# Optimization experiments

Measured on AMD Instinct MI355X. Metric: run time of the kernel, lower is better.

## Reference

```python
import jax, jax.numpy as jnp
import numpy as np

B, S, D, H, E, K = 1, 2048, 1024, 16, 8, 2
DK = D // H          # 64 per-head key dim
FF = 4 * D           # 4096 expert hidden
EPS = 1e-5


def rmsnorm(x, scale):
    rms = jnp.sqrt(jnp.mean(x * x, axis=-1, keepdims=True) + EPS)
    return scale * (x / rms)


def setup_inputs() -> dict:
    key = jax.random.key(0)
    ks = jax.random.split(key, 12)
    std = 0.02
    x = jax.random.normal(ks[0], (B, S, D), dtype=jnp.float32)
    # causal mask: masked_fill where mask == 0
    self_attn_mask = jnp.tril(jnp.ones((S, S), dtype=jnp.int32))
    scale_attn = jnp.ones((D,), dtype=jnp.float32)
    scale_ffn = jnp.ones((D,), dtype=jnp.float32)
    # per-head projections, stacked: [H, DK, D] (torch Linear weight layout [out,in])
    Wq = jax.random.normal(ks[1], (H, DK, D), dtype=jnp.float32) * std
    Wk = jax.random.normal(ks[2], (H, DK, D), dtype=jnp.float32) * std
    Wv = jax.random.normal(ks[3], (H, DK, D), dtype=jnp.float32) * std
    Wo = jax.random.normal(ks[4], (D, D), dtype=jnp.float32) * std
    Wg = jax.random.normal(ks[5], (E, D), dtype=jnp.float32) * std   # router gate
    W_in = jax.random.normal(ks[6], (E, FF, D), dtype=jnp.float32) * std   # expert linear
    W_v = jax.random.normal(ks[7], (E, FF, D), dtype=jnp.float32) * std    # expert linear_v
    W_out = jax.random.normal(ks[8], (E, D, FF), dtype=jnp.float32) * std  # expert linear_out
    return {
        'x': x, 'self_attn_mask': self_attn_mask,
        'scale_attn': scale_attn, 'Wq': Wq, 'Wk': Wk, 'Wv': Wv, 'Wo': Wo,
        'scale_ffn': scale_ffn, 'Wg': Wg, 'W_in': W_in, 'W_v': W_v, 'W_out': W_out,
    }


def reference(x, self_attn_mask, scale_attn, Wq, Wk, Wv, Wo, scale_ffn, Wg, W_in, W_v, W_out):
    # --- self attention (pre-RMSNorm) ---
    normed = rmsnorm(x, scale_attn)
    q = jnp.einsum('bsd,hkd->bhsk', normed, Wq)
    k = jnp.einsum('bsd,hkd->bhsk', normed, Wk)
    v = jnp.einsum('bsd,hkd->bhsk', normed, Wv)
    attn = jnp.einsum('bhsk,bhtk->bhst', q, k) / np.sqrt(DK).astype(np.float32)
    attn = jnp.where(self_attn_mask[None, None] == 0, -jnp.inf, attn)
    attn = jax.nn.softmax(attn, axis=-1)
    ctx = jnp.einsum('bhst,bhtk->bhsk', attn, v)
    ctx = ctx.transpose(0, 2, 1, 3).reshape(x.shape[0], x.shape[1], D)  # concat heads
    a1 = ctx @ Wo.T
    x = x + a1
    # --- MoE (pre-RMSNorm) ---
    normed = rmsnorm(x, scale_ffn)
    router_logits = normed @ Wg.T                       # [B,S,E]
    router_probs = jax.nn.softmax(router_logits, axis=-1)
    gate, idx = jax.lax.top_k(router_probs, K)          # [B,S,K]
    gate = gate / jnp.sum(gate, axis=-1, keepdims=True)
    # combine weights per expert: sum of renormalized gates over selected slots
    onehot = (idx[..., None] == jnp.arange(E)).astype(x.dtype)  # [B,S,K,E]
    combine = jnp.sum(gate[..., None] * onehot, axis=2)         # [B,S,E]
    # all-expert dense FFN (faithful to the masked dense loop in torch)
    g = jax.nn.gelu(jnp.einsum('bsd,efd->bsef', normed, W_in), approximate=False)
    val = jnp.einsum('bsd,efd->bsef', normed, W_v)
    eo = jnp.einsum('bsef,edf->bsed', g * val, W_out)           # [B,S,E,D]
    moe_out = jnp.einsum('bse,bsed->bsd', combine, eo)
    out = x + moe_out
    return (out, router_probs)
```

## Files before the change

### kernel.cpp

```cpp
#include <hip/hip_runtime.h>
#include <hip/hip_bf16.h>
#include <math.h>

typedef unsigned int u32;
typedef unsigned short u16;
using bf16x8 = __attribute__((ext_vector_type(8))) short;
using f32x4 = __attribute__((ext_vector_type(4))) float;

#define MFMA_BF16(a, b, c) __builtin_amdgcn_mfma_f32_16x16x32_bf16((a), (b), (c), 0, 0, 0)
#define VMCNT8() asm volatile("s_waitcnt vmcnt(8)" ::: "memory")
#define VMCNT6() asm volatile("s_waitcnt vmcnt(6)" ::: "memory")
#define VMCNT4() asm volatile("s_waitcnt vmcnt(4)" ::: "memory")
#define VMCNT0() asm volatile("s_waitcnt vmcnt(0)" ::: "memory")
#define SBAR() __builtin_amdgcn_s_barrier()
#define SCHED0() __builtin_amdgcn_sched_barrier(0)

constexpr int kS = 2048, kD = 1024, kH = 16, kE = 8, kFF = 4096;
constexpr int kSlotCap = 5120;
constexpr int kMaxTiles = 40;
constexpr int kChunk = 8;

__device__ __forceinline__ u16 bf16_rne(float f) {
  u32 u = __float_as_uint(f);
  u32 r = (u + 0x7fffu + ((u >> 16) & 1u)) >> 16;
  return (u16)r;
}
__device__ __forceinline__ float bf16_f32(u16 h) { return __uint_as_float(((u32)h) << 16); }
__device__ __forceinline__ u32 pack_hl(float x) {
  u16 hi = bf16_rne(x);
  u16 lo = bf16_rne(x - bf16_f32(hi));
  return ((u32)lo << 16) | (u32)hi;
}
__device__ __forceinline__ void unpack8(const u32* t, bf16x8& h, bf16x8& l) {
#pragma unroll
  for (int j = 0; j < 8; j++) {
    h[j] = (short)(t[j] & 0xffffu);
    l[j] = (short)(t[j] >> 16);
  }
}
__device__ __forceinline__ void gload_lds16(const void* g, void* l) {
  __builtin_amdgcn_global_load_lds((const __attribute__((address_space(1))) u32*)g,
                                   (__attribute__((address_space(3))) u32*)l, 16, 0, 0);
}
__device__ __forceinline__ u32 cvtpk(float a, float b) {
  u32 r;
  asm("v_cvt_pk_bf16_f32 %0, %1, %2" : "=v"(r) : "v"(a), "v"(b));
  return r;
}

__global__ __launch_bounds__(256) void pack_dp3(const float* __restrict__ Wq,
                                                const float* __restrict__ Wk,
                                                const float* __restrict__ Wv,
                                                u16* __restrict__ o) {
  int i = blockIdx.x * 256 + threadIdx.x;
  if (i >= 3072 * 1024) return;
  int n = i >> 10, k = i & 1023;
  float v = (n < 1024) ? Wq[i] : (n < 2048) ? Wk[i - 1024 * 1024] : Wv[i - 2048 * 1024];
  u16 hi = bf16_rne(v);
  u16 lo = bf16_rne(v - bf16_f32(hi));
  size_t b = (size_t)n * 2048 + (size_t)(k >> 5) * 64 + (k & 31);
  o[b] = hi;
  o[b + 32] = lo;
}
__global__ __launch_bounds__(256) void pack_dp1(const float* __restrict__ W,
                                                u16* __restrict__ o, int n_elem) {
  int i = blockIdx.x * 256 + threadIdx.x;
  if (i >= n_elem) return;
  int k = i & 1023, n = i >> 10;
  float v = W[i];
  u16 hi = bf16_rne(v);
  u16 lo = bf16_rne(v - bf16_f32(hi));
  size_t b = (size_t)n * 2048 + (size_t)(k >> 5) * 64 + (k & 31);
  o[b] = hi;
  o[b + 32] = lo;
}

template <int MODE>
__global__ __launch_bounds__(256) void rmsnorm_kernel(
    const float* __restrict__ x, const float* __restrict__ scale,
    u16* __restrict__ odp, float* __restrict__ of32, u16* __restrict__ ob16) {
  const int s = blockIdx.x;
  const float* row = x + (size_t)s * kD;
  const int c = threadIdx.x * 4;
  float4 v = *(const float4*)(row + c);
  float ss = v.x * v.x + v.y * v.y + v.z * v.z + v.w * v.w;
#pragma unroll
  for (int m = 32; m; m >>= 1) ss += __shfl_xor(ss, m);
  __shared__ float wsum[4];
  if ((threadIdx.x & 63) == 0) wsum[threadIdx.x >> 6] = ss;
  __syncthreads();
  float tot = wsum[0] + wsum[1] + wsum[2] + wsum[3];
  float rinv = 1.0f / sqrtf(tot * (1.0f / kD) + 1e-5f);
  float4 sc = *(const float4*)(scale + c);
  float n[4] = {v.x * rinv * sc.x, v.y * rinv * sc.y, v.z * rinv * sc.z, v.w * rinv * sc.w};
  if (MODE == 0) {
    u16 hv[4], lv[4];
#pragma unroll
    for (int j = 0; j < 4; j++) {
      hv[j] = bf16_rne(n[j]);
      lv[j] = bf16_rne(n[j] - bf16_f32(hv[j]));
    }
    u16* o = odp + (size_t)s * 2048 + (size_t)(c >> 5) * 64 + (c & 31);
    *(uint2*)o = *(uint2*)hv;
    *(uint2*)(o + 32) = *(uint2*)lv;
  } else {
    *(float4*)(of32 + (size_t)s * kD + c) = make_float4(n[0], n[1], n[2], n[3]);
    u16* o = ob16 + (size_t)s * kD + c;
    o[0] = bf16_rne(n[0]); o[1] = bf16_rne(n[1]); o[2] = bf16_rne(n[2]); o[3] = bf16_rne(n[3]);
  }
}

template <int APK, int OUT>
__global__ __launch_bounds__(256) void gemm_dp(
    const void* __restrict__ Av, const u16* __restrict__ Bdp,
    const float* __restrict__ resid, int K,
    u32* __restrict__ oq, u32* __restrict__ ok, u32* __restrict__ ov,
    float* __restrict__ of) {
  __shared__ u16 As[2][128 * 64];
  __shared__ u16 Bs[2][128 * 64];
  const int tid = threadIdx.x, w = tid >> 6, l = tid & 63;
  const int m0 = blockIdx.y * 128, n0 = blockIdx.x * 128;
  const int wr = (w >> 1) * 64, wc = (w & 1) * 64;
  const char* Ab = (const char*)Av;
  const char* Bb = (const char*)Bdp;
  const size_t rowb = (size_t)K * 4;

  size_t asrc[4], bsrc[4];
  int dst[4];
#pragma unroll
  for (int i = 0; i < 4; i++) {
    int fl = i * 256 + tid;
    int row = fl >> 3, cb = fl & 7;
    size_t coff = (size_t)((cb ^ (row & 7)) * 16);
    asrc[i] = (size_t)(m0 + row) * rowb + coff;
    bsrc[i] = (size_t)(n0 + row) * rowb + coff;
    dst[i] = fl * 16;
  }

  f32x4 zero = {0.f, 0.f, 0.f, 0.f};
  f32x4 acc[4][4];
#pragma unroll
  for (int i = 0; i < 4; i++)
#pragma unroll
    for (int j = 0; j < 4; j++) acc[i][j] = zero;

  auto stage = [&](int buf, int s) {
    const char* ap = Ab + (size_t)s * 128;
    const char* bp = Bb + (size_t)s * 128;
#pragma unroll
    for (int i = 0; i < 4; i++) {
      gload_lds16(ap + asrc[i], (char*)&As[buf][0] + dst[i]);
      gload_lds16(bp + bsrc[i], (char*)&Bs[buf][0] + dst[i]);
    }
  };

  const int NS = K / 32;
  stage(0, 0);
  for (int s = 0; s < NS; s++) {
    const int cur = s & 1;
    const bool lastit = (s == NS - 1);
    if (!lastit) stage(cur ^ 1, s + 1);
    if (!lastit) VMCNT8(); else VMCNT0();
    SBAR();
    SCHED0();
    bf16x8 ah[4], al[4], bh[4], bl[4];
    const int g = l >> 4;
    if (APK) {
      const u32* At = (const u32*)&As[cur][0];
#pragma unroll
      for (int mi = 0; mi < 4; mi++) {
        int row = wr + mi * 16 + (l & 15);
        u32 t[8];
        *(uint4*)t = *(const uint4*)&At[row * 32 + (((2 * g) ^ (row & 7)) * 4)];
        *(uint4*)(t + 4) = *(const uint4*)&At[row * 32 + (((2 * g + 1) ^ (row & 7)) * 4)];
        unpack8(t, ah[mi], al[mi]);
      }
    } else {
#pragma unroll
      for (int mi = 0; mi < 4; mi++) {
        int row = wr + mi * 16 + (l & 15);
        ah[mi] = *(const bf16x8*)&As[cur][row * 64 + ((g ^ (row & 7)) * 8)];
        al[mi] = *(const bf16x8*)&As[cur][row * 64 + (((4 + g) ^ (row & 7)) * 8)];
      }
    }
#pragma unroll
    for (int ni = 0; ni < 4; ni++) {
      int row = wc + ni * 16 + (l & 15);
      bh[ni] = *(const bf16x8*)&Bs[cur][row * 64 + ((g ^ (row & 7)) * 8)];
      bl[ni] = *(const bf16x8*)&Bs[cur][row * 64 + (((4 + g) ^ (row & 7)) * 8)];
    }
#pragma unroll
    for (int mi = 0; mi < 4; mi++)
#pragma unroll
      for (int ni = 0; ni < 4; ni++) {
        f32x4 c = acc[mi][ni];
        c = MFMA_BF16(al[mi], bh[ni], c);
        c = MFMA_BF16(ah[mi], bl[ni], c);
        c = MFMA_BF16(ah[mi], bh[ni], c);
        acc[mi][ni] = c;
      }
    SCHED0();
    if (!lastit) SBAR();
  }

  if (OUT == 0) {
    u32* dstp;
    int nb;
    if (n0 < 1024) { dstp = oq; nb = n0; }
    else if (n0 < 2048) { dstp = ok; nb = n0 - 1024; }
    else { dstp = ov; nb = n0 - 2048; }
#pragma unroll
    for (int mi = 0; mi < 4; mi++)
#pragma unroll
      for (int ni = 0; ni < 4; ni++)
#pragma unroll
        for (int r = 0; r < 4; r++) {
          int row = m0 + wr + mi * 16 + ((l >> 4) << 2) + r;
          int col = nb + wc + ni * 16 + (l & 15);
          dstp[(size_t)row * 1024 + col] = pack_hl(acc[mi][ni][r]);
        }
  } else {
#pragma unroll
    for (int mi = 0; mi < 4; mi++)
#pragma unroll
      for (int ni = 0; ni < 4; ni++)
#pragma unroll
        for (int r = 0; r < 4; r++) {
          int row = m0 + wr + mi * 16 + ((l >> 4) << 2) + r;
          int col = n0 + wc + ni * 16 + (l & 15);
          of[(size_t)row * 1024 + col] = resid[(size_t)row * 1024 + col] + acc[mi][ni][r];
        }
  }
}

__global__ __launch_bounds__(256) void attn_kernel(
    const u32* __restrict__ Qp, const u32* __restrict__ Kp, const u32* __restrict__ Vp,
    float* __restrict__ Opart, float* __restrict__ mpart, float* __restrict__ lpart) {
  constexpr int LDK = 68;
  __shared__ u32 Ks[64 * LDK];
  __shared__ u32 Vs[64 * LDK];
  __shared__ u32 Ps[64 * LDK];
  const int tid = threadIdx.x, w = tid >> 6, l = tid & 63;
  int b = blockIdx.x, qt, c;
  if (b < 8) { qt = b; c = 0; }
  else if (b < 24) { qt = 8 + ((b - 8) >> 1); c = (b - 8) & 1; }
  else if (b < 48) { qt = 16 + (b - 24) / 3; c = (b - 24) % 3; }
  else { qt = 24 + ((b - 48) >> 2); c = (b - 48) & 3; }
  const int hh = blockIdx.y;
  const int q0 = qt * 64, hc = hh * 64;
  const int kt0 = c * kChunk;
  const int kt1 = min(kt0 + kChunk, qt + 1);

  bf16x8 qh[2], ql[2];
  {
    const int qrow = q0 + w * 16 + (l & 15);
#pragma unroll
    for (int kk = 0; kk < 2; kk++) {
      u32 t[8];
      const u32* p = Qp + (size_t)qrow * kD + hc + kk * 32 + ((l >> 4) << 3);
      *(uint4*)t = *(const uint4*)p;
      *(uint4*)(t + 4) = *(const uint4*)(p + 4);
      unpack8(t, qh[kk], ql[kk]);
    }
  }
  float mrun[4], lrun[4];
  f32x4 zero = {0.f, 0.f, 0.f, 0.f};
  f32x4 oacc[4];
#pragma unroll
  for (int r = 0; r < 4; r++) { mrun[r] = -3.0e38f; lrun[r] = 0.f; }
#pragma unroll
  for (int vb = 0; vb < 4; vb++) oacc[vb] = zero;

  const int trow = tid >> 2, c0v = (tid & 3) * 16;
  const u32* gKb = Kp + hc + c0v;
  const u32* gVb = Vp + hc + c0v;
  uint4 kr[4], vr[4];
  {
    const u32* gK = gKb + (size_t)(kt0 * 64 + trow) * kD;
    kr[0] = *(const uint4*)gK; kr[1] = *(const uint4*)(gK + 4);
    kr[2] = *(const uint4*)(gK + 8); kr[3] = *(const uint4*)(gK + 12);
    const u32* gV = gVb + (size_t)(kt0 * 64 + trow) * kD;
    vr[0] = *(const uint4*)gV; vr[1] = *(const uint4*)(gV + 4);
    vr[2] = *(const uint4*)(gV + 8); vr[3] = *(const uint4*)(gV + 12);
  }

  for (int kt = kt0; kt < kt1; kt++) {
    {
      u32* sK = Ks + trow * LDK + c0v;
      *(uint4*)sK = kr[0]; *(uint4*)(sK + 4) = kr[1];
      *(uint4*)(sK + 8) = kr[2]; *(uint4*)(sK + 12) = kr[3];
#pragma unroll
      for (int j = 0; j < 4; j++) {
        Vs[(c0v + j * 4 + 0) * LDK + trow] = vr[j].x;
        Vs[(c0v + j * 4 + 1) * LDK + trow] = vr[j].y;
        Vs[(c0v + j * 4 + 2) * LDK + trow] = vr[j].z;
        Vs[(c0v + j * 4 + 3) * LDK + trow] = vr[j].w;
      }
    }
    __syncthreads();
    if (kt + 1 < kt1) {
      const u32* gK = gKb + (size_t)((kt + 1) * 64 + trow) * kD;
      kr[0] = *(const uint4*)gK; kr[1] = *(const uint4*)(gK + 4);
      kr[2] = *(const uint4*)(gK + 8); kr[3] = *(const uint4*)(gK + 12);
      const u32* gV = gVb + (size_t)((kt + 1) * 64 + trow) * kD;
      vr[0] = *(const uint4*)gV; vr[1] = *(const uint4*)(gV + 4);
      vr[2] = *(const uint4*)(gV + 8); vr[3] = *(const uint4*)(gV + 12);
    }

    f32x4 sfr[4];
#pragma unroll
    for (int kb = 0; kb < 4; kb++) {
      f32x4 sa = zero;
#pragma unroll
      for (int kk = 0; kk < 2; kk++) {
        u32 t[8];
        bf16x8 kh, kl;
        const u32* p = Ks + (kb * 16 + (l & 15)) * LDK + kk * 32 + ((l >> 4) << 3);
        *(uint4*)t = *(const uint4*)p;
        *(uint4*)(t + 4) = *(const uint4*)(p + 4);
        unpack8(t, kh, kl);
        sa = MFMA_BF16(ql[kk], kl, sa);
        sa = MFMA_BF16(ql[kk], kh, sa);
        sa = MFMA_BF16(qh[kk], kl, sa);
        sa = MFMA_BF16(qh[kk], kh, sa);
      }
      sfr[kb] = sa * 0.125f;
    }
    if (kt == qt) {
#pragma unroll
      for (int kb = 0; kb < 4; kb++) {
        int t = kt * 64 + kb * 16 + (l & 15);
#pragma unroll
        for (int r = 0; r < 4; r++) {
          int qq = q0 + w * 16 + ((l >> 4) << 2) + r;
          if (t > qq) sfr[kb][r] = -3.0e38f;
        }
      }
    }
#pragma unroll
    for (int r = 0; r < 4; r++) {
      float mx = fmaxf(fmaxf(sfr[0][r], sfr[1][r]), fmaxf(sfr[2][r], sfr[3][r]));
#pragma unroll
      for (int mm = 1; mm < 16; mm <<= 1) mx = fmaxf(mx, __shfl_xor(mx, mm));
      float mnew = fmaxf(mrun[r], mx);
      float sf = __expf(mrun[r] - mnew);
      mrun[r] = mnew;
      float rs = 0.f;
#pragma unroll
      for (int kb = 0; kb < 4; kb++) {
        float p = __expf(sfr[kb][r] - mnew);
        sfr[kb][r] = p;
        rs += p;
      }
#pragma unroll
      for (int mm = 1; mm < 16; mm <<= 1) rs += __shfl_xor(rs, mm);
      lrun[r] = lrun[r] * sf + rs;
#pragma unroll
      for (int vb = 0; vb < 4; vb++) oacc[vb][r] *= sf;
    }
#pragma unroll
    for (int kb = 0; kb < 4; kb++)
#pragma unroll
      for (int r = 0; r < 4; r++)
        Ps[(w * 16 + ((l >> 4) << 2) + r) * LDK + kb * 16 + (l & 15)] = pack_hl(sfr[kb][r]);
#pragma unroll
    for (int ks = 0; ks < 2; ks++) {
      bf16x8 ph, pl;
      {
        u32 t[8];
        const u32* pp = Ps + (w * 16 + (l & 15)) * LDK + ks * 32 + ((l >> 4) << 3);
        *(uint4*)t = *(const uint4*)pp;
        *(uint4*)(t + 4) = *(const uint4*)(pp + 4);
        unpack8(t, ph, pl);
      }
#pragma unroll
      for (int vb = 0; vb < 4; vb++) {
        u32 t2[8];
        bf16x8 vh, vl;
        const u32* pv = Vs + (vb * 16 + (l & 15)) * LDK + ks * 32 + ((l >> 4) << 3);
        *(uint4*)t2 = *(const uint4*)pv;
        *(uint4*)(t2 + 4) = *(const uint4*)(pv + 4);
        unpack8(t2, vh, vl);
        f32x4 cc = oacc[vb];
        cc = MFMA_BF16(pl, vl, cc);
        cc = MFMA_BF16(pl, vh, cc);
        cc = MFMA_BF16(ph, vl, cc);
        cc = MFMA_BF16(ph, vh, cc);
        oacc[vb] = cc;
      }
    }
    __syncthreads();
  }

  const int p = (qt * 16 + hh) * 4 + c;
  float* Po = Opart + (size_t)p * 4096;
#pragma unroll
  for (int vb = 0; vb < 4; vb++)
#pragma unroll
    for (int r = 0; r < 4; r++) {
      int rl = w * 16 + ((l >> 4) << 2) + r;
      int cl = vb * 16 + (l & 15);
      Po[rl * 64 + cl] = oacc[vb][r];
    }
  if ((l & 15) == 0) {
#pragma unroll
    for (int r = 0; r < 4; r++) {
      int rl = w * 16 + ((l >> 4) << 2) + r;
      mpart[p * 64 + rl] = mrun[r];
      lpart[p * 64 + rl] = lrun[r];
    }
  }
}

__global__ __launch_bounds__(256) void attn_merge(
    const float* __restrict__ Opart, const float* __restrict__ mpart,
    const float* __restrict__ lpart, u32* __restrict__ Op) {
  const int qt = blockIdx.x, hh = blockIdx.y;
  const int nch = (qt + kChunk) >> 3;
  const int t = threadIdx.x;
  const int row = t >> 2;
  const int c0 = (t & 3) * 16;
  const int pbase = (qt * 16 + hh) * 4;
  float M = -3.0e38f;
  for (int c = 0; c < nch; c++) M = fmaxf(M, mpart[(pbase + c) * 64 + row]);
  float den = 0.f;
  float acc[16];
#pragma unroll
  for (int j = 0; j < 16; j++) acc[j] = 0.f;
  for (int c = 0; c < nch; c++) {
    float wgt = __expf(mpart[(pbase + c) * 64 + row] - M);
    den += wgt * lpart[(pbase + c) * 64 + row];
    const float* po = Opart + (size_t)(pbase + c) * 4096 + row * 64 + c0;
#pragma unroll
    for (int j = 0; j < 16; j += 4) {
      float4 v = *(const float4*)(po + j);
      acc[j] += wgt * v.x; acc[j + 1] += wgt * v.y;
      acc[j + 2] += wgt * v.z; acc[j + 3] += wgt * v.w;
    }
  }
  float inv = 1.f / den;
  u32* dst = Op + (size_t)(qt * 64 + row) * kD + hh * 64 + c0;
#pragma unroll
  for (int j = 0; j < 16; j++) dst[j] = pack_hl(acc[j] * inv);
}

__global__ __launch_bounds__(256) void router_kernel(
    const float* __restrict__ normed, const float* __restrict__ Wg,
    float* __restrict__ probs, float* __restrict__ gates,
    int* __restrict__ experts, int* __restrict__ counts) {
  const int w = threadIdx.x >> 6, l = threadIdx.x & 63;
  const int s = blockIdx.x * 4 + w;
  float lg[kE];
  const float* row = normed + (size_t)s * kD;
#pragma unroll
  for (int e = 0; e < kE; e++) {
    const float* wg = Wg + (size_t)e * kD;
    float a = 0.f;
    for (int d = l; d < kD; d += 64) a += row[d] * wg[d];
#pragma unroll
    for (int m = 32; m; m >>= 1) a += __shfl_xor(a, m);
    lg[e] = a;
  }
  if (l == 0) {
    float mx = lg[0];
#pragma unroll
    for (int e = 1; e < kE; e++) mx = fmaxf(mx, lg[e]);
    float p[kE], sum = 0.f;
#pragma unroll
    for (int e = 0; e < kE; e++) { p[e] = __expf(lg[e] - mx); sum += p[e]; }
    float inv = 1.f / sum;
#pragma unroll
    for (int e = 0; e < kE; e++) { p[e] *= inv; probs[(size_t)s * kE + e] = p[e]; }
    int i1 = 0;
#pragma unroll
    for (int e = 1; e < kE; e++) if (lg[e] > lg[i1]) i1 = e;
    int i2 = (i1 == 0) ? 1 : 0;
#pragma unroll
    for (int e = 0; e < kE; e++) if (e != i1 && lg[e] > lg[i2]) i2 = e;
    float den = 1.f / (p[i1] + p[i2]);
    gates[s * 2] = p[i1] * den;
    gates[s * 2 + 1] = p[i2] * den;
    experts[s * 2] = i1;
    experts[s * 2 + 1] = i2;
    atomicAdd(&counts[i1], 1);
    atomicAdd(&counts[i2], 1);
  }
}

__global__ void moe_init(int* counts) {
  if (threadIdx.x < kE) counts[threadIdx.x] = 0;
}
__global__ void moe_scan(const int* __restrict__ counts, int* __restrict__ ebase,
                         int* __restrict__ cursor, int2* __restrict__ tmap) {
  if (threadIdx.x == 0) {
    int acc = 0, t = 0;
    for (int e = 0; e < kE; e++) {
      ebase[e] = acc;
      cursor[e] = acc;
      int nt = (counts[e] + 127) >> 7;
      for (int i = 0; i < nt; i++) tmap[t++] = make_int2(e, i * 128);
      acc += nt << 7;
    }
    ebase[kE] = acc;
    for (; t < kMaxTiles; t++) tmap[t] = make_int2(-1, 0);
  }
}
__global__ void moe_fill(const int* __restrict__ experts, int* __restrict__ cursor,
                         int* __restrict__ slot_list, int* __restrict__ slot_of) {
  int s = blockIdx.x * 256 + threadIdx.x;
  if (s >= kS) return;
  for (int k = 0; k < 2; k++) {
    int e = experts[s * 2 + k];
    int pos = atomicAdd(&cursor[e], 1);
    slot_list[pos] = s;
    slot_of[s * 2 + k] = pos;
  }
}

__global__ __launch_bounds__(256) void moe_mmA(
    const u16* __restrict__ A, const float* __restrict__ Wi, const float* __restrict__ Wv2,
    const int* __restrict__ slot_list, const int* __restrict__ counts,
    const int* __restrict__ ebase, const int2* __restrict__ tmap,
    u16* __restrict__ H) {
  int2 tm = tmap[blockIdx.y];
  const int e = tm.x;
  if (e < 0) return;
  const int base = ebase[e], Me = counts[e], m0 = tm.y;
  const int n0 = blockIdx.x * 128;
  __shared__ u16 As[2][64 * 64];
  __shared__ float Bsf[2][128 * 32];
  const int tid = threadIdx.x, w = tid >> 6, l = tid & 63;
  const int wr = (w >> 1) * 64, wc = (w & 1) * 64;
  const char* Ab = (const char*)A;

  size_t asrc[2];
  int adst[2];
#pragma unroll
  for (int i = 0; i < 2; i++) {
    int fl = i * 256 + tid;
    int lrow = fl >> 3, sl = fl & 7;
    int sp = sl ^ (lrow & 7);
    int t = 2 * lrow + (sp >> 2);
    int cbl = sp & 3;
    int mr = m0 + t;
    if (mr > Me - 1) mr = Me - 1;
    int ar = slot_list[base + mr];
    asrc[i] = (size_t)ar * 2048 + (size_t)cbl * 16;
    adst[i] = fl * 16;
  }
  const char* bptr[4];
  int bdst[4];
#pragma unroll
  for (int i = 0; i < 4; i++) {
    int fl = i * 256 + tid;
    int row = fl >> 3, sl = fl & 7;
    int sp = sl ^ (row & 7);
    int nn = n0 + row;
    const float* srcT = (nn & 1) ? Wv2 : Wi;
    bptr[i] = (const char*)(srcT + ((size_t)e * 4096 + (nn >> 1)) * 1024) + sp * 16;
    bdst[i] = fl * 16;
  }

  const int g = l >> 4;
  int aoff[4], boff0[4], boff1[4];
#pragma unroll
  for (int mi = 0; mi < 4; mi++) {
    int t = wr + mi * 16 + (l & 15);
    int lr = t >> 1;
    int sl = (((t & 1) << 2) | g) ^ (lr & 7);
    aoff[mi] = lr * 128 + sl * 16;
  }
#pragma unroll
  for (int ni = 0; ni < 4; ni++) {
    int rr = wc + ni * 16 + (l & 15);
    boff0[ni] = rr * 128 + (((2 * g) ^ (rr & 7)) * 16);
    boff1[ni] = rr * 128 + (((2 * g + 1) ^ (rr & 7)) * 16);
  }

  f32x4 zero = {0.f, 0.f, 0.f, 0.f};
  f32x4 acc[4][4];
#pragma unroll
  for (int i = 0; i < 4; i++)
#pragma unroll
    for (int j = 0; j < 4; j++) acc[i][j] = zero;

  auto stage = [&](int buf, int s) {
    const size_t soA = (size_t)s * 64;
    const size_t soB = (size_t)s * 128;
#pragma unroll
    for (int i = 0; i < 2; i++)
      gload_lds16(Ab + soA + asrc[i], (char*)&As[buf][0] + adst[i]);
#pragma unroll
    for (int i = 0; i < 4; i++)
      gload_lds16(bptr[i] + soB, (char*)&Bsf[buf][0] + bdst[i]);
  };

  const int NS = kD / 32;
  stage(0, 0);
  for (int s = 0; s < NS; s++) {
    const int cur = s & 1;
    const bool lastit = (s == NS - 1);
    if (!lastit) stage(cur ^ 1, s + 1);
    if (!lastit) VMCNT6(); else VMCNT0();
    SBAR();
    SCHED0();
    const char* Ac = (const char*)&As[cur][0];
    const char* Bc = (const char*)&Bsf[cur][0];
    bf16x8 af[4], bfr[4];
#pragma unroll
    for (int mi = 0; mi < 4; mi++) af[mi] = *(const bf16x8*)(Ac + aoff[mi]);
#pragma unroll
    for (int ni = 0; ni < 4; ni++) {
      float4 f0 = *(const float4*)(Bc + boff0[ni]);
      float4 f1 = *(const float4*)(Bc + boff1[ni]);
      u32 pk[4];
      pk[0] = cvtpk(f0.x, f0.y);
      pk[1] = cvtpk(f0.z, f0.w);
      pk[2] = cvtpk(f1.x, f1.y);
      pk[3] = cvtpk(f1.z, f1.w);
      bfr[ni] = *(bf16x8*)pk;
    }
#pragma unroll
    for (int mi = 0; mi < 4; mi++)
#pragma unroll
      for (int ni = 0; ni < 4; ni++) acc[mi][ni] = MFMA_BF16(af[mi], bfr[ni], acc[mi][ni]);
    SCHED0();
    if (!lastit) SBAR();
  }

#pragma unroll
  for (int mi = 0; mi < 4; mi++)
#pragma unroll
    for (int r = 0; r < 4; r++) {
      int ml = m0 + wr + mi * 16 + ((l >> 4) << 2) + r;
      if (ml >= Me) continue;
      size_t rb = (size_t)(base + ml) * 4096;
#pragma unroll
      for (int ni = 0; ni < 4; ni++) {
        int col = n0 + wc + ni * 16 + (l & 15);
        float v0 = acc[mi][ni][r];
        float pv = __shfl_xor(v0, 1);
        if ((l & 1) == 0) {
          float ge = 0.5f * v0 * (1.0f + erff(v0 * 0.70710678118654752f));
          H[rb + (col >> 1)] = bf16_rne(ge * pv);
        }
      }
    }
}

__global__ __launch_bounds__(256) void moe_mm2(
    const u16* __restrict__ H, const float* __restrict__ Wo_f,
    const int* __restrict__ counts, const int* __restrict__ ebase,
    const int2* __restrict__ tmap, float* __restrict__ eo) {
  int2 tm = tmap[blockIdx.y];
  const int e = tm.x;
  if (e < 0) return;
  const int base = ebase[e], Me = counts[e], m0 = tm.y;
  const int n0 = blockIdx.x * 64;
  __shared__ u16 As[2][64 * 64];
  __shared__ float Bsf[2][64 * 32];
  const int tid = threadIdx.x, w = tid >> 6, l = tid & 63;
  const int wr = (w >> 1) * 64, wc = (w & 1) * 32;
  const char* Ab = (const char*)H;

  size_t asrc[2];
  int adst[2];
#pragma unroll
  for (int i = 0; i < 2; i++) {
    int fl = i * 256 + tid;
    int lrow = fl >> 3, sl = fl & 7;
    int sp = sl ^ (lrow & 7);
    int t = 2 * lrow + (sp >> 2);
    int cbl = sp & 3;
    int mr = m0 + t;
    if (mr > Me - 1) mr = Me - 1;
    asrc[i] = (size_t)(base + mr) * 8192 + (size_t)cbl * 16;
    adst[i] = fl * 16;
  }
  const char* bptr[2];
  int bdst[2];
#pragma unroll
  for (int i = 0; i < 2; i++) {
    int fl = i * 256 + tid;
    int row = fl >> 3, sl = fl & 7;
    int sp = sl ^ (row & 7);
    bptr[i] = (const char*)(Wo_f + ((size_t)e * 1024 + n0 + row) * 4096) + sp * 16;
    bdst[i] = fl * 16;
  }

  const int g = l >> 4;
  int aoff[4], boff0[2], boff1[2];
#pragma unroll
  for (int mi = 0; mi < 4; mi++) {
    int t = wr + mi * 16 + (l & 15);
    int lr = t >> 1;
    int sl = (((t & 1) << 2) | g) ^ (lr & 7);
    aoff[mi] = lr * 128 + sl * 16;
  }
#pragma unroll
  for (int ni = 0; ni < 2; ni++) {
    int rr = wc + ni * 16 + (l & 15);
    boff0[ni] = rr * 128 + (((2 * g) ^ (rr & 7)) * 16);
    boff1[ni] = rr * 128 + (((2 * g + 1) ^ (rr & 7)) * 16);
  }

  f32x4 zero = {0.f, 0.f, 0.f, 0.f};
  f32x4 acc[4][2];
#pragma unroll
  for (int i = 0; i < 4; i++)
#pragma unroll
    for (int j = 0; j < 2; j++) acc[i][j] = zero;

  auto stage = [&](int buf, int s) {
    const size_t soA = (size_t)s * 64;
    const size_t soB = (size_t)s * 128;
#pragma unroll
    for (int i = 0; i < 2; i++)
      gload_lds16(Ab + soA + asrc[i], (char*)&As[buf][0] + adst[i]);
#pragma unroll
    for (int i = 0; i < 2; i++)
      gload_lds16(bptr[i] + soB, (char*)&Bsf[buf][0] + bdst[i]);
  };

  const int NS = kFF / 32;
  stage(0, 0);
  for (int s = 0; s < NS; s++) {
    const int cur = s & 1;
    const bool lastit = (s == NS - 1);
    if (!lastit) stage(cur ^ 1, s + 1);
    if (!lastit) VMCNT4(); else VMCNT0();
    SBAR();
    SCHED0();
    const char* Ac = (const char*)&As[cur][0];
    const char* Bc = (const char*)&Bsf[cur][0];
    bf16x8 af[4], bfr[2];
#pragma unroll
    for (int mi = 0; mi < 4; mi++) af[mi] = *(const bf16x8*)(Ac + aoff[mi]);
#pragma unroll
    for (int ni = 0; ni < 2; ni++) {
      float4 f0 = *(const float4*)(Bc + boff0[ni]);
      float4 f1 = *(const float4*)(Bc + boff1[ni]);
      u32 pk[4];
      pk[0] = cvtpk(f0.x, f0.y);
      pk[1] = cvtpk(f0.z, f0.w);
      pk[2] = cvtpk(f1.x, f1.y);
      pk[3] = cvtpk(f1.z, f1.w);
      bfr[ni] = *(bf16x8*)pk;
    }
#pragma unroll
    for (int mi = 0; mi < 4; mi++)
#pragma unroll
      for (int ni = 0; ni < 2; ni++) acc[mi][ni] = MFMA_BF16(af[mi], bfr[ni], acc[mi][ni]);
    SCHED0();
    if (!lastit) SBAR();
  }

#pragma unroll
  for (int mi = 0; mi < 4; mi++)
#pragma unroll
    for (int r = 0; r < 4; r++) {
      int ml = m0 + wr + mi * 16 + ((l >> 4) << 2) + r;
      if (ml >= Me) continue;
      size_t rb = (size_t)(base + ml) * kD;
#pragma unroll
      for (int ni = 0; ni < 2; ni++) {
        int col = n0 + wc + ni * 16 + (l & 15);
        eo[rb + col] = acc[mi][ni][r];
      }
    }
}

__global__ __launch_bounds__(256) void combine_kernel(
    const float* __restrict__ h, const float* __restrict__ eo,
    const float* __restrict__ gates, const int* __restrict__ slot_of,
    float* __restrict__ out) {
  const int s = blockIdx.x;
  const float g0 = gates[s * 2], g1 = gates[s * 2 + 1];
  const int p0 = slot_of[s * 2], p1 = slot_of[s * 2 + 1];
  const int c = threadIdx.x * 4;
  float4 hv = *(const float4*)(h + (size_t)s * kD + c);
  float4 e0 = *(const float4*)(eo + (size_t)p0 * kD + c);
  float4 e1 = *(const float4*)(eo + (size_t)p1 * kD + c);
  float4 o;
  o.x = hv.x + g0 * e0.x + g1 * e1.x;
  o.y = hv.y + g0 * e0.y + g1 * e1.y;
  o.z = hv.z + g0 * e0.z + g1 * e1.z;
  o.w = hv.w + g0 * e0.w + g1 * e1.w;
  *(float4*)(out + (size_t)s * kD + c) = o;
}

extern "C" void kernel_launch(void* const* d_in, const int* in_sizes, int n_in,
                              void* d_out, int out_size, void* d_ws, size_t ws_size,
                              hipStream_t stream) {
  (void)in_sizes; (void)n_in; (void)out_size; (void)ws_size;
  const float* x = (const float*)d_in[0];
  const float* scale_attn = (const float*)d_in[2];
  const float* Wq = (const float*)d_in[3];
  const float* Wk = (const float*)d_in[4];
  const float* Wv = (const float*)d_in[5];
  const float* Wo = (const float*)d_in[6];
  const float* scale_ffn = (const float*)d_in[7];
  const float* Wg = (const float*)d_in[8];
  const float* W_in = (const float*)d_in[9];
  const float* W_vv = (const float*)d_in[10];
  const float* W_out = (const float*)d_in[11];
  float* out = (float*)d_out;
  float* probs = out + (size_t)kS * kD;

  char* wsb = (char*)d_ws;
  size_t off = 0;
  auto alloc = [&](size_t bytes) -> void* {
    void* p = wsb + off;
    off += (bytes + 255) & ~(size_t)255;
    return p;
  };
  const size_t SDu = (size_t)kS * kD;
  u16* normA_dp = (u16*)alloc(SDu * 4);
  u32* qpk = (u32*)alloc(SDu * 4);
  u32* kpk = (u32*)alloc(SDu * 4);
  u32* vpk = (u32*)alloc(SDu * 4);
  u32* ctxpk = (u32*)alloc(SDu * 4);
  u16* Wqkv_dp = (u16*)alloc((size_t)3072 * 2048 * 2);
  u16* Wo_dp = (u16*)alloc((size_t)1024 * 2048 * 2);
  float* normFf = (float*)alloc(SDu * 4);
  float* eo = (float*)alloc((size_t)kSlotCap * kD * 4);
  float* h = (float*)alloc(SDu * 4);
  u16* normFb = (u16*)alloc(SDu * 2);
  u16* H = (u16*)alloc((size_t)kSlotCap * kFF * 2);
  float* Opart = (float*)alloc((size_t)2048 * 4096 * 4);
  float* mpart = (float*)alloc((size_t)2048 * 64 * 4);
  float* lpart = (float*)alloc((size_t)2048 * 64 * 4);
  float* gates = (float*)alloc(kS * 2 * 4);
  int* experts = (int*)alloc(kS * 2 * 4);
  int* slot_of = (int*)alloc(kS * 2 * 4);
  int* slot_list = (int*)alloc(kSlotCap * 4);
  int* counts = (int*)alloc(64);
  int* ebase = (int*)alloc(64);
  int* cursor = (int*)alloc(64);
  int2* tmap = (int2*)alloc(kMaxTiles * 8);

  pack_dp3<<<(3072 * 1024) / 256, 256, 0, stream>>>(Wq, Wk, Wv, Wqkv_dp);
  pack_dp1<<<(1024 * 1024) / 256, 256, 0, stream>>>(Wo, Wo_dp, 1024 * 1024);

  rmsnorm_kernel<0><<<kS, 256, 0, stream>>>(x, scale_attn, normA_dp, nullptr, nullptr);
  gemm_dp<0, 0><<<dim3(3072 / 128, kS / 128), 256, 0, stream>>>(
      normA_dp, Wqkv_dp, nullptr, kD, qpk, kpk, vpk, nullptr);
  attn_kernel<<<dim3(80, kH), 256, 0, stream>>>(qpk, kpk, vpk, Opart, mpart, lpart);
  attn_merge<<<dim3(kS / 64, kH), 256, 0, stream>>>(Opart, mpart, lpart, ctxpk);
  gemm_dp<1, 1><<<dim3(1024 / 128, kS / 128), 256, 0, stream>>>(
      ctxpk, Wo_dp, x, kD, nullptr, nullptr, nullptr, h);

  rmsnorm_kernel<1><<<kS, 256, 0, stream>>>(h, scale_ffn, nullptr, normFf, normFb);
  moe_init<<<1, 64, 0, stream>>>(counts);
  router_kernel<<<kS / 4, 256, 0, stream>>>(normFf, Wg, probs, gates, experts, counts);
  moe_scan<<<1, 64, 0, stream>>>(counts, ebase, cursor, tmap);
  moe_fill<<<kS / 256, 256, 0, stream>>>(experts, cursor, slot_list, slot_of);

  moe_mmA<<<dim3(8192 / 128, kMaxTiles), 256, 0, stream>>>(
      normFb, W_in, W_vv, slot_list, counts, ebase, tmap, H);
  moe_mm2<<<dim3(kD / 64, kMaxTiles), 256, 0, stream>>>(
      H, W_out, counts, ebase, tmap, eo);

  combine_kernel<<<kS, 256, 0, stream>>>(h, eo, gates, slot_of, out);
}
```

Before: 625.1 us.

## Register-prefetch and pre-convert expert weights to bf16 before LDS staging in MoE GEMMs

Both MoE GEMM kernels stop using direct global-to-LDS async loads of fp32 weights. Each thread now loads the next K-slice into registers, runs the MFMAs on the current LDS buffer, then converts the fp32 weights to bf16 and writes them into a swizzled bf16 LDS tile. This halves the LDS footprint and bandwidth for B and removes the repeated per-wave fp32-to-bf16 conversion after LDS reads. In exchange it adds register pressure and gives up the async LDS-load path, so global-load latency must now be hidden by the MFMA work between the load and the store.

Measured after the change: 626.1 us. Within noise of the previous version (+0.2%).

```diff
diff --git a/kernel.cpp b/kernel.cpp
--- a/kernel.cpp
+++ b/kernel.cpp
@@ -9,9 +9,8 @@
 
 #define MFMA_BF16(a, b, c) __builtin_amdgcn_mfma_f32_16x16x32_bf16((a), (b), (c), 0, 0, 0)
 #define VMCNT8() asm volatile("s_waitcnt vmcnt(8)" ::: "memory")
-#define VMCNT6() asm volatile("s_waitcnt vmcnt(6)" ::: "memory")
-#define VMCNT4() asm volatile("s_waitcnt vmcnt(4)" ::: "memory")
 #define VMCNT0() asm volatile("s_waitcnt vmcnt(0)" ::: "memory")
+#define LGKM0() asm volatile("s_waitcnt lgkmcnt(0)" ::: "memory")
 #define SBAR() __builtin_amdgcn_s_barrier()
 #define SCHED0() __builtin_amdgcn_sched_barrier(0)
 
@@ -528,53 +527,35 @@
   const int base = ebase[e], Me = counts[e], m0 = tm.y;
   const int n0 = blockIdx.x * 128;
   __shared__ u16 As[2][64 * 64];
-  __shared__ float Bsf[2][128 * 32];
+  __shared__ u16 Bs[2][64 * 64];
   const int tid = threadIdx.x, w = tid >> 6, l = tid & 63;
   const int wr = (w >> 1) * 64, wc = (w & 1) * 64;
-  const char* Ab = (const char*)A;
-
-  size_t asrc[2];
-  int adst[2];
-#pragma unroll
-  for (int i = 0; i < 2; i++) {
-    int fl = i * 256 + tid;
-    int lrow = fl >> 3, sl = fl & 7;
-    int sp = sl ^ (lrow & 7);
-    int t = 2 * lrow + (sp >> 2);
-    int cbl = sp & 3;
-    int mr = m0 + t;
-    if (mr > Me - 1) mr = Me - 1;
-    int ar = slot_list[base + mr];
-    asrc[i] = (size_t)ar * 2048 + (size_t)cbl * 16;
-    adst[i] = fl * 16;
-  }
-  const char* bptr[4];
-  int bdst[4];
-#pragma unroll
-  for (int i = 0; i < 4; i++) {
-    int fl = i * 256 + tid;
-    int row = fl >> 3, sl = fl & 7;
-    int sp = sl ^ (row & 7);
-    int nn = n0 + row;
-    const float* srcT = (nn & 1) ? Wv2 : Wi;
-    bptr[i] = (const char*)(srcT + ((size_t)e * 4096 + (nn >> 1)) * 1024) + sp * 16;
-    bdst[i] = fl * 16;
-  }
+
+  const int srow = tid >> 1, sh = tid & 1;
+  int mrA = m0 + srow;
+  if (mrA > Me - 1) mrA = Me - 1;
+  const int arow = slot_list[base + mrA];
+  const u16* agp = A + (size_t)arow * 1024 + sh * 16;
+  const int nn = n0 + srow;
+  const float* srcT = (nn & 1) ? Wv2 : Wi;
+  const float* bgp = srcT + ((size_t)e * 4096 + (nn >> 1)) * 1024 + sh * 16;
+  const int wl = srow >> 1;
+  const int awo0 = wl * 128 + (((((srow & 1) << 2) | (sh * 2)) ^ (wl & 7)) * 16);
+  const int awo1 = wl * 128 + (((((srow & 1) << 2) | (sh * 2 + 1)) ^ (wl & 7)) * 16);
 
   const int g = l >> 4;
-  int aoff[4], boff0[4], boff1[4];
+  int aoff[4], boff[4];
 #pragma unroll
   for (int mi = 0; mi < 4; mi++) {
     int t = wr + mi * 16 + (l & 15);
     int lr = t >> 1;
-    int sl = (((t & 1) << 2) | g) ^ (lr & 7);
-    aoff[mi] = lr * 128 + sl * 16;
+    aoff[mi] = lr * 128 + (((((t & 1) << 2) | g) ^ (lr & 7)) * 16);
   }
 #pragma unroll
   for (int ni = 0; ni < 4; ni++) {
-    int rr = wc + ni * 16 + (l & 15);
-    boff0[ni] = rr * 128 + (((2 * g) ^ (rr & 7)) * 16);
-    boff1[ni] = rr * 128 + (((2 * g + 1) ^ (rr & 7)) * 16);
+    int t = wc + ni * 16 + (l & 15);
+    int lr = t >> 1;
+    boff[ni] = lr * 128 + (((((t & 1) << 2) | g) ^ (lr & 7)) * 16);
   }
 
   f32x4 zero = {0.f, 0.f, 0.f, 0.f};
@@ -584,48 +565,69 @@
 #pragma unroll
     for (int j = 0; j < 4; j++) acc[i][j] = zero;
 
-  auto stage = [&](int buf, int s) {
-    const size_t soA = (size_t)s * 64;
-    const size_t soB = (size_t)s * 128;
-#pragma unroll
-    for (int i = 0; i < 2; i++)
-      gload_lds16(Ab + soA + asrc[i], (char*)&As[buf][0] + adst[i]);
-#pragma unroll
-    for (int i = 0; i < 4; i++)
-      gload_lds16(bptr[i] + soB, (char*)&Bsf[buf][0] + bdst[i]);
-  };
+  uint4 a0 = *(const uint4*)agp;
+  uint4 a1 = *(const uint4*)(agp + 8);
+  float4 b0 = *(const float4*)bgp;
+  float4 b1 = *(const float4*)(bgp + 4);
+  float4 b2 = *(const float4*)(bgp + 8);
+  float4 b3 = *(const float4*)(bgp + 12);
+  {
+    *(uint4*)((char*)&As[0][0] + awo0) = a0;
+    *(uint4*)((char*)&As[0][0] + awo1) = a1;
+    u32 pk[4];
+    pk[0] = cvtpk(b0.x, b0.y); pk[1] = cvtpk(b0.z, b0.w);
+    pk[2] = cvtpk(b1.x, b1.y); pk[3] = cvtpk(b1.z, b1.w);
+    *(uint4*)((char*)&Bs[0][0] + awo0) = *(uint4*)pk;
+    pk[0] = cvtpk(b2.x, b2.y); pk[1] = cvtpk(b2.z, b2.w);
+    pk[2] = cvtpk(b3.x, b3.y); pk[3] = cvtpk(b3.z, b3.w);
+    *(uint4*)((char*)&Bs[0][0] + awo1) = *(uint4*)pk;
+  }
+  LGKM0();
+  SBAR();
+  SCHED0();
 
   const int NS = kD / 32;
-  stage(0, 0);
   for (int s = 0; s < NS; s++) {
     const int cur = s & 1;
-    const bool lastit = (s == NS - 1);
-    if (!lastit) stage(cur ^ 1, s + 1);
-    if (!lastit) VMCNT6(); else VMCNT0();
-    SBAR();
+    const bool more = (s + 1 < NS);
+    if (more) {
+      const u16* ap = agp + (s + 1) * 32;
+      a0 = *(const uint4*)ap;
+      a1 = *(const uint4*)(ap + 8);
+      const float* bp = bgp + (s + 1) * 32;
+      b0 = *(const float4*)bp;
+      b1 = *(const float4*)(bp + 4);
+      b2 = *(const float4*)(bp + 8);
+      b3 = *(const float4*)(bp + 12);
+    }
     SCHED0();
     const char* Ac = (const char*)&As[cur][0];
-    const char* Bc = (const char*)&Bsf[cur][0];
+    const char* Bc = (const char*)&Bs[cur][0];
     bf16x8 af[4], bfr[4];
 #pragma unroll
     for (int mi = 0; mi < 4; mi++) af[mi] = *(const bf16x8*)(Ac + aoff[mi]);
 #pragma unroll
-    for (int ni = 0; ni < 4; ni++) {
-      float4 f0 = *(const float4*)(Bc + boff0[ni]);
-      float4 f1 = *(const float4*)(Bc + boff1[ni]);
+    for (int ni = 0; ni < 4; ni++) bfr[ni] = *(const bf16x8*)(Bc + boff[ni]);
+#pragma unroll
+    for (int mi = 0; mi < 4; mi++)
+#pragma unroll
+      for (int ni = 0; ni < 4; ni++) acc[mi][ni] = MFMA_BF16(af[mi], bfr[ni], acc[mi][ni]);
+    if (more) {
+      char* Aw = (char*)&As[cur ^ 1][0];
+      char* Bw = (char*)&Bs[cur ^ 1][0];
+      *(uint4*)(Aw + awo0) = a0;
+      *(uint4*)(Aw + awo1) = a1;
       u32 pk[4];
-      pk[0] = cvtpk(f0.x, f0.y);
-      pk[1] = cvtpk(f0.z, f0.w);
-      pk[2] = cvtpk(f1.x, f1.y);
-      pk[3] = cvtpk(f1.z, f1.w);
-      bfr[ni] = *(bf16x8*)pk;
-    }
-#pragma unroll
-    for (int mi = 0; mi < 4; mi++)
-#pragma unroll
-      for (int ni = 0; ni < 4; ni++) acc[mi][ni] = MFMA_BF16(af[mi], bfr[ni], acc[mi][ni]);
-    SCHED0();
-    if (!lastit) SBAR();
+      pk[0] = cvtpk(b0.x, b0.y); pk[1] = cvtpk(b0.z, b0.w);
+      pk[2] = cvtpk(b1.x, b1.y); pk[3] = cvtpk(b1.z, b1.w);
+      *(uint4*)(Bw + awo0) = *(uint4*)pk;
+      pk[0] = cvtpk(b2.x, b2.y); pk[1] = cvtpk(b2.z, b2.w);
+      pk[2] = cvtpk(b3.x, b3.y); pk[3] = cvtpk(b3.z, b3.w);
+      *(uint4*)(Bw + awo1) = *(uint4*)pk;
+      LGKM0();
+      SBAR();
+      SCHED0();
+    }
   }
 
 #pragma unroll
@@ -658,50 +660,35 @@
   const int base = ebase[e], Me = counts[e], m0 = tm.y;
   const int n0 = blockIdx.x * 64;
   __shared__ u16 As[2][64 * 64];
-  __shared__ float Bsf[2][64 * 32];
+  __shared__ u16 Bs[2][32 * 64];
   const int tid = threadIdx.x, w = tid >> 6, l = tid & 63;
   const int wr = (w >> 1) * 64, wc = (w & 1) * 32;
-  const char* Ab = (const char*)H;
-
-  size_t asrc[2];
-  int adst[2];
-#pragma unroll
-  for (int i = 0; i < 2; i++) {
-    int fl = i * 256 + tid;
-    int lrow = fl >> 3, sl = fl & 7;
-    int sp = sl ^ (lrow & 7);
-    int t = 2 * lrow + (sp >> 2);
-    int cbl = sp & 3;
-    int mr = m0 + t;
-    if (mr > Me - 1) mr = Me - 1;
-    asrc[i] = (size_t)(base + mr) * 8192 + (size_t)cbl * 16;
-    adst[i] = fl * 16;
-  }
-  const char* bptr[2];
-  int bdst[2];
-#pragma unroll
-  for (int i = 0; i < 2; i++) {
-    int fl = i * 256 + tid;
-    int row = fl >> 3, sl = fl & 7;
-    int sp = sl ^ (row & 7);
-    bptr[i] = (const char*)(Wo_f + ((size_t)e * 1024 + n0 + row) * 4096) + sp * 16;
-    bdst[i] = fl * 16;
-  }
+
+  const int srow = tid >> 1, sh = tid & 1;
+  int mrA = m0 + srow;
+  if (mrA > Me - 1) mrA = Me - 1;
+  const u16* agp = H + (size_t)(base + mrA) * 4096 + sh * 16;
+  const int wlA = srow >> 1;
+  const int awo0 = wlA * 128 + (((((srow & 1) << 2) | (sh * 2)) ^ (wlA & 7)) * 16);
+  const int awo1 = wlA * 128 + (((((srow & 1) << 2) | (sh * 2 + 1)) ^ (wlA & 7)) * 16);
+  const int brow = tid >> 2, bq = tid & 3;
+  const float* bgp = Wo_f + ((size_t)e * 1024 + n0 + brow) * 4096 + bq * 8;
+  const int wlB = brow >> 1;
+  const int bwo = wlB * 128 + (((((brow & 1) << 2) | bq) ^ (wlB & 7)) * 16);
 
   const int g = l >> 4;
-  int aoff[4], boff0[2], boff1[2];
+  int aoff[4], boff[2];
 #pragma unroll
   for (int mi = 0; mi < 4; mi++) {
     int t = wr + mi * 16 + (l & 15);
     int lr = t >> 1;
-    int sl = (((t & 1) << 2) | g) ^ (lr & 7);
-    aoff[mi] = lr * 128 + sl * 16;
+    aoff[mi] = lr * 128 + (((((t & 1) << 2) | g) ^ (lr & 7)) * 16);
   }
 #pragma unroll
   for (int ni = 0; ni < 2; ni++) {
-    int rr = wc + ni * 16 + (l & 15);
-    boff0[ni] = rr * 128 + (((2 * g) ^ (rr & 7)) * 16);
-    boff1[ni] = rr * 128 + (((2 * g + 1) ^ (rr & 7)) * 16);
+    int t = wc + ni * 16 + (l & 15);
+    int lr = t >> 1;
+    boff[ni] = lr * 128 + (((((t & 1) << 2) | g) ^ (lr & 7)) * 16);
   }
 
   f32x4 zero = {0.f, 0.f, 0.f, 0.f};
@@ -711,48 +698,59 @@
 #pragma unroll
     for (int j = 0; j < 2; j++) acc[i][j] = zero;
 
-  auto stage = [&](int buf, int s) {
-    const size_t soA = (size_t)s * 64;
-    const size_t soB = (size_t)s * 128;
-#pragma unroll
-    for (int i = 0; i < 2; i++)
-      gload_lds16(Ab + soA + asrc[i], (char*)&As[buf][0] + adst[i]);
-#pragma unroll
-    for (int i = 0; i < 2; i++)
-      gload_lds16(bptr[i] + soB, (char*)&Bsf[buf][0] + bdst[i]);
-  };
+  uint4 a0 = *(const uint4*)agp;
+  uint4 a1 = *(const uint4*)(agp + 8);
+  float4 b0 = *(const float4*)bgp;
+  float4 b1 = *(const float4*)(bgp + 4);
+  {
+    *(uint4*)((char*)&As[0][0] + awo0) = a0;
+    *(uint4*)((char*)&As[0][0] + awo1) = a1;
+    u32 pk[4];
+    pk[0] = cvtpk(b0.x, b0.y); pk[1] = cvtpk(b0.z, b0.w);
+    pk[2] = cvtpk(b1.x, b1.y); pk[3] = cvtpk(b1.z, b1.w);
+    *(uint4*)((char*)&Bs[0][0] + bwo) = *(uint4*)pk;
+  }
+  LGKM0();
+  SBAR();
+  SCHED0();
 
   const int NS = kFF / 32;
-  stage(0, 0);
   for (int s = 0; s < NS; s++) {
     const int cur = s & 1;
-    const bool lastit = (s == NS - 1);
-    if (!lastit) stage(cur ^ 1, s + 1);
-    if (!lastit) VMCNT4(); else VMCNT0();
-    SBAR();
+    const bool more = (s + 1 < NS);
+    if (more) {
+      const u16* ap = agp + (s + 1) * 32;
+      a0 = *(const uint4*)ap;
+      a1 = *(const uint4*)(ap + 8);
+      const float* bp = bgp + (s + 1) * 32;
+      b0 = *(const float4*)bp;
+      b1 = *(const float4*)(bp + 4);
+    }
     SCHED0();
     const char* Ac = (const char*)&As[cur][0];
-    const char* Bc = (const char*)&Bsf[cur][0];
+    const char* Bc = (const char*)&Bs[cur][0];
     bf16x8 af[4], bfr[2];
 #pragma unroll
     for (int mi = 0; mi < 4; mi++) af[mi] = *(const bf16x8*)(Ac + aoff[mi]);
 #pragma unroll
-    for (int ni = 0; ni < 2; ni++) {
-      float4 f0 = *(const float4*)(Bc + boff0[ni]);
-      float4 f1 = *(const float4*)(Bc + boff1[ni]);
+    for (int ni = 0; ni < 2; ni++) bfr[ni] = *(const bf16x8*)(Bc + boff[ni]);
+#pragma unroll
+    for (int mi = 0; mi < 4; mi++)
+#pragma unroll
+      for (int ni = 0; ni < 2; ni++) acc[mi][ni] = MFMA_BF16(af[mi], bfr[ni], acc[mi][ni]);
+    if (more) {
+      char* Aw = (char*)&As[cur ^ 1][0];
+      char* Bw = (char*)&Bs[cur ^ 1][0];
+      *(uint4*)(Aw + awo0) = a0;
+      *(uint4*)(Aw + awo1) = a1;
       u32 pk[4];
-      pk[0] = cvtpk(f0.x, f0.y);
-      pk[1] = cvtpk(f0.z, f0.w);
-      pk[2] = cvtpk(f1.x, f1.y);
-      pk[3] = cvtpk(f1.z, f1.w);
-      bfr[ni] = *(bf16x8*)pk;
-    }
-#pragma unroll
-    for (int mi = 0; mi < 4; mi++)
-#pragma unroll
-      for (int ni = 0; ni < 2; ni++) acc[mi][ni] = MFMA_BF16(af[mi], bfr[ni], acc[mi][ni]);
-    SCHED0();
-    if (!lastit) SBAR();
+      pk[0] = cvtpk(b0.x, b0.y); pk[1] = cvtpk(b0.z, b0.w);
+      pk[2] = cvtpk(b1.x, b1.y); pk[3] = cvtpk(b1.z, b1.w);
+      *(uint4*)(Bw + bwo) = *(uint4*)pk;
+      LGKM0();
+      SBAR();
+      SCHED0();
+    }
   }
 
 #pragma unroll
```

## Stage MoE down-projection tiles through registers with bf16 conversion before LDS

Applied to the files above, without the earlier changes.

The moe_mm2 kernel no longer uses direct global-to-LDS async loads. It now loads the next A and B tiles into registers, converts the fp32 expert weights to bf16 once at store time, and writes them to a swizzled bf16 LDS buffer after the current MFMAs. This halves the B tile's LDS footprint and removes redundant per-wave conversions, and it cuts one barrier per iteration. In exchange, global load latency has to be hidden by the MFMA work of a single stage, and register pressure goes up.

Result: faster. 611.6 us (median of 3 runs) (-2.2%).

```diff
diff --git a/kernel.cpp b/kernel.cpp
--- a/kernel.cpp
+++ b/kernel.cpp
@@ -10,8 +10,8 @@
 #define MFMA_BF16(a, b, c) __builtin_amdgcn_mfma_f32_16x16x32_bf16((a), (b), (c), 0, 0, 0)
 #define VMCNT8() asm volatile("s_waitcnt vmcnt(8)" ::: "memory")
 #define VMCNT6() asm volatile("s_waitcnt vmcnt(6)" ::: "memory")
-#define VMCNT4() asm volatile("s_waitcnt vmcnt(4)" ::: "memory")
 #define VMCNT0() asm volatile("s_waitcnt vmcnt(0)" ::: "memory")
+#define LGKM0() asm volatile("s_waitcnt lgkmcnt(0)" ::: "memory")
 #define SBAR() __builtin_amdgcn_s_barrier()
 #define SCHED0() __builtin_amdgcn_sched_barrier(0)
 
@@ -658,50 +658,35 @@
   const int base = ebase[e], Me = counts[e], m0 = tm.y;
   const int n0 = blockIdx.x * 64;
   __shared__ u16 As[2][64 * 64];
-  __shared__ float Bsf[2][64 * 32];
+  __shared__ u16 Bs[2][32 * 64];
   const int tid = threadIdx.x, w = tid >> 6, l = tid & 63;
   const int wr = (w >> 1) * 64, wc = (w & 1) * 32;
-  const char* Ab = (const char*)H;
-
-  size_t asrc[2];
-  int adst[2];
-#pragma unroll
-  for (int i = 0; i < 2; i++) {
-    int fl = i * 256 + tid;
-    int lrow = fl >> 3, sl = fl & 7;
-    int sp = sl ^ (lrow & 7);
-    int t = 2 * lrow + (sp >> 2);
-    int cbl = sp & 3;
-    int mr = m0 + t;
-    if (mr > Me - 1) mr = Me - 1;
-    asrc[i] = (size_t)(base + mr) * 8192 + (size_t)cbl * 16;
-    adst[i] = fl * 16;
-  }
-  const char* bptr[2];
-  int bdst[2];
-#pragma unroll
-  for (int i = 0; i < 2; i++) {
-    int fl = i * 256 + tid;
-    int row = fl >> 3, sl = fl & 7;
-    int sp = sl ^ (row & 7);
-    bptr[i] = (const char*)(Wo_f + ((size_t)e * 1024 + n0 + row) * 4096) + sp * 16;
-    bdst[i] = fl * 16;
-  }
+
+  const int srow = tid >> 1, sh = tid & 1;
+  int mrA = m0 + srow;
+  if (mrA > Me - 1) mrA = Me - 1;
+  const u16* agp = H + (size_t)(base + mrA) * 4096 + sh * 16;
+  const int wlA = srow >> 1;
+  const int awo0 = wlA * 128 + (((((srow & 1) << 2) | (sh * 2)) ^ (wlA & 7)) * 16);
+  const int awo1 = wlA * 128 + (((((srow & 1) << 2) | (sh * 2 + 1)) ^ (wlA & 7)) * 16);
+  const int brow = tid >> 2, bq = tid & 3;
+  const float* bgp = Wo_f + ((size_t)e * 1024 + n0 + brow) * 4096 + bq * 8;
+  const int wlB = brow >> 1;
+  const int bwo = wlB * 128 + (((((brow & 1) << 2) | bq) ^ (wlB & 7)) * 16);
 
   const int g = l >> 4;
-  int aoff[4], boff0[2], boff1[2];
+  int aoff[4], boff[2];
 #pragma unroll
   for (int mi = 0; mi < 4; mi++) {
     int t = wr + mi * 16 + (l & 15);
     int lr = t >> 1;
-    int sl = (((t & 1) << 2) | g) ^ (lr & 7);
-    aoff[mi] = lr * 128 + sl * 16;
+    aoff[mi] = lr * 128 + (((((t & 1) << 2) | g) ^ (lr & 7)) * 16);
   }
 #pragma unroll
   for (int ni = 0; ni < 2; ni++) {
-    int rr = wc + ni * 16 + (l & 15);
-    boff0[ni] = rr * 128 + (((2 * g) ^ (rr & 7)) * 16);
-    boff1[ni] = rr * 128 + (((2 * g + 1) ^ (rr & 7)) * 16);
+    int t = wc + ni * 16 + (l & 15);
+    int lr = t >> 1;
+    boff[ni] = lr * 128 + (((((t & 1) << 2) | g) ^ (lr & 7)) * 16);
   }
 
   f32x4 zero = {0.f, 0.f, 0.f, 0.f};
@@ -711,48 +696,59 @@
 #pragma unroll
     for (int j = 0; j < 2; j++) acc[i][j] = zero;
 
-  auto stage = [&](int buf, int s) {
-    const size_t soA = (size_t)s * 64;
-    const size_t soB = (size_t)s * 128;
-#pragma unroll
-    for (int i = 0; i < 2; i++)
-      gload_lds16(Ab + soA + asrc[i], (char*)&As[buf][0] + adst[i]);
-#pragma unroll
-    for (int i = 0; i < 2; i++)
-      gload_lds16(bptr[i] + soB, (char*)&Bsf[buf][0] + bdst[i]);
-  };
+  uint4 a0 = *(const uint4*)agp;
+  uint4 a1 = *(const uint4*)(agp + 8);
+  float4 b0 = *(const float4*)bgp;
+  float4 b1 = *(const float4*)(bgp + 4);
+  {
+    *(uint4*)((char*)&As[0][0] + awo0) = a0;
+    *(uint4*)((char*)&As[0][0] + awo1) = a1;
+    u32 pk[4];
+    pk[0] = cvtpk(b0.x, b0.y); pk[1] = cvtpk(b0.z, b0.w);
+    pk[2] = cvtpk(b1.x, b1.y); pk[3] = cvtpk(b1.z, b1.w);
+    *(uint4*)((char*)&Bs[0][0] + bwo) = *(uint4*)pk;
+  }
+  LGKM0();
+  SBAR();
+  SCHED0();
 
   const int NS = kFF / 32;
-  stage(0, 0);
   for (int s = 0; s < NS; s++) {
     const int cur = s & 1;
-    const bool lastit = (s == NS - 1);
-    if (!lastit) stage(cur ^ 1, s + 1);
-    if (!lastit) VMCNT4(); else VMCNT0();
-    SBAR();
+    const bool more = (s + 1 < NS);
+    if (more) {
+      const u16* ap = agp + (s + 1) * 32;
+      a0 = *(const uint4*)ap;
+      a1 = *(const uint4*)(ap + 8);
+      const float* bp = bgp + (s + 1) * 32;
+      b0 = *(const float4*)bp;
+      b1 = *(const float4*)(bp + 4);
+    }
     SCHED0();
     const char* Ac = (const char*)&As[cur][0];
-    const char* Bc = (const char*)&Bsf[cur][0];
+    const char* Bc = (const char*)&Bs[cur][0];
     bf16x8 af[4], bfr[2];
 #pragma unroll
     for (int mi = 0; mi < 4; mi++) af[mi] = *(const bf16x8*)(Ac + aoff[mi]);
 #pragma unroll
-    for (int ni = 0; ni < 2; ni++) {
-      float4 f0 = *(const float4*)(Bc + boff0[ni]);
-      float4 f1 = *(const float4*)(Bc + boff1[ni]);
+    for (int ni = 0; ni < 2; ni++) bfr[ni] = *(const bf16x8*)(Bc + boff[ni]);
+#pragma unroll
+    for (int mi = 0; mi < 4; mi++)
+#pragma unroll
+      for (int ni = 0; ni < 2; ni++) acc[mi][ni] = MFMA_BF16(af[mi], bfr[ni], acc[mi][ni]);
+    if (more) {
+      char* Aw = (char*)&As[cur ^ 1][0];
+      char* Bw = (char*)&Bs[cur ^ 1][0];
+      *(uint4*)(Aw + awo0) = a0;
+      *(uint4*)(Aw + awo1) = a1;
       u32 pk[4];
-      pk[0] = cvtpk(f0.x, f0.y);
-      pk[1] = cvtpk(f0.z, f0.w);
-      pk[2] = cvtpk(f1.x, f1.y);
-      pk[3] = cvtpk(f1.z, f1.w);
-      bfr[ni] = *(bf16x8*)pk;
-    }
-#pragma unroll
-    for (int mi = 0; mi < 4; mi++)
-#pragma unroll
-      for (int ni = 0; ni < 2; ni++) acc[mi][ni] = MFMA_BF16(af[mi], bfr[ni], acc[mi][ni]);
-    SCHED0();
-    if (!lastit) SBAR();
+      pk[0] = cvtpk(b0.x, b0.y); pk[1] = cvtpk(b0.z, b0.w);
+      pk[2] = cvtpk(b1.x, b1.y); pk[3] = cvtpk(b1.z, b1.w);
+      *(uint4*)(Bw + bwo) = *(uint4*)pk;
+      LGKM0();
+      SBAR();
+      SCHED0();
+    }
   }
 
 #pragma unroll
```
